# Kernel optimization log

Measured on AMD Instinct MI355X. Metric: run time of the kernel, lower is better.

The kernel has to match this reference:

```python
import jax, jax.numpy as jnp
import numpy as np

N_NODES = 100000
N_EDGES = 1200000
DIM = 64


def _gcn_layer(h, src, dst, norm, W, b):
    # GCNConv: linear -> gather -> normalize -> scatter-add -> bias
    n = h.shape[0]
    h = h @ W                              # [N, D]
    msg = h[src] * norm[:, None]           # [E+N, D] gathered edge messages
    out = jax.ops.segment_sum(msg, dst, num_segments=n)
    return out + b


def setup_inputs() -> dict:
    key = jax.random.key(0)
    ks = jax.random.split(key, 8)
    s = 1.0 / np.sqrt(DIM)
    return {
        "x": jax.random.normal(ks[0], (N_NODES, DIM), jnp.float32),
        "edge_index": jax.random.randint(ks[1], (2, N_EDGES), 0, N_NODES, dtype=jnp.int32),
        "W1": jax.random.normal(ks[2], (DIM, DIM), jnp.float32) * s,
        "b1": jnp.zeros((DIM,), jnp.float32),
        "W2": jax.random.normal(ks[3], (DIM, DIM), jnp.float32) * s,
        "b2": jnp.zeros((DIM,), jnp.float32),
        "W3": jax.random.normal(ks[4], (DIM, DIM), jnp.float32) * s,
        "b3": jnp.zeros((DIM,), jnp.float32),
    }


def reference(x, edge_index, W1, b1, W2, b2, W3, b3):
    n = x.shape[0]
    loops = jnp.arange(n, dtype=edge_index.dtype)
    src = jnp.concatenate([edge_index[0], loops])   # add self-loops (PyG GCNConv default)
    dst = jnp.concatenate([edge_index[1], loops])
    # symmetric degree normalization: norm_e = d^-1/2[src] * d^-1/2[dst]
    deg = jax.ops.segment_sum(jnp.ones(src.shape, x.dtype), dst, num_segments=n)
    dinv = jnp.where(deg > 0, jax.lax.rsqrt(deg), 0.0)
    norm = dinv[src] * dinv[dst]
    h = jax.nn.relu(_gcn_layer(x, src, dst, norm, W1, b1))   # dropout inactive at eval
    h = jax.nn.relu(_gcn_layer(h, src, dst, norm, W2, b2))
    return _gcn_layer(h, src, dst, norm, W3, b3)
```

## Files before the change

kernel.cpp:

```cpp
#include <hip/hip_runtime.h>
#include <math.h>

#define N_NODES 100000
#define N_EDGES 1200000
#define DIM 64
#define ELL_STRIDE 48
#define BNODES 128
#define NBUCKET ((N_NODES + BNODES - 1) / BNODES)
#define BIN_SHIFT 10
#define NBIN ((N_NODES + 1023) >> 10)
#define BIN_CAP 16384
#define CAP 40
#define BIN_BLOCKS 512
#define EPB ((N_EDGES + BIN_BLOCKS - 1) / BIN_BLOCKS)
#define GEMM_BLOCKS ((N_NODES + 63) / 64)

__device__ __forceinline__ unsigned short f2bf(float f) {
    union { float f; unsigned int u; } v; v.f = f;
    unsigned int r = v.u + 0x7FFF + ((v.u >> 16) & 1);
    return (unsigned short)(r >> 16);
}
__device__ __forceinline__ float bf2f(unsigned short us) {
    return __uint_as_float((unsigned int)us << 16);
}


__global__ void k_init(int* __restrict__ tail) {
    if (threadIdx.x < NBIN) tail[threadIdx.x * 16] = 0;
}


__device__ __forceinline__ void gemm_block(int bid, const float* __restrict__ x,
                                           const float* __restrict__ W,
                                           unsigned short* __restrict__ h,
                                           float4* __restrict__ Xlds) {
    const int tid = threadIdx.x;
    const int lane = tid & 63;

    float wreg[64];
#pragma unroll
    for (int k = 0; k < 64; ++k) wreg[k] = W[k * DIM + lane];

    const int base = bid * 64;
#pragma unroll
    for (int it = 0; it < 4; ++it) {
        int f = tid + it * 256;
        int row = base + (f >> 4);
        if (row >= N_NODES) row = N_NODES - 1;
        Xlds[f] = ((const float4*)x)[row * 16 + (f & 15)];
    }
    __syncthreads();

    const int m0 = (tid >> 6) * 16;
    for (int m = 0; m < 16; ++m) {
        const float4* xr = &Xlds[(m0 + m) * 16];
        float a0 = 0.f, a1 = 0.f, a2 = 0.f, a3 = 0.f;
#pragma unroll
        for (int k4 = 0; k4 < 16; ++k4) {
            float4 xv = xr[k4];
            a0 = fmaf(xv.x, wreg[k4 * 4 + 0], a0);
            a1 = fmaf(xv.y, wreg[k4 * 4 + 1], a1);
            a2 = fmaf(xv.z, wreg[k4 * 4 + 2], a2);
            a3 = fmaf(xv.w, wreg[k4 * 4 + 3], a3);
        }
        int row = base + m0 + m;
        if (row < N_NODES)
            h[(size_t)row * DIM + lane] = f2bf((a0 + a1) + (a2 + a3));
    }
}


__global__ void __launch_bounds__(256) k_pre(const int* __restrict__ ei,
                                             const float* __restrict__ x,
                                             const float* __restrict__ W1,
                                             int* __restrict__ tail,
                                             int2* __restrict__ part,
                                             unsigned short* __restrict__ h) {
    __shared__ __align__(16) char smraw[NBIN * CAP * 8];
    __shared__ int lcnt[NBIN];
    __shared__ int gbase[NBIN];
    __shared__ int gcnt[NBIN];

    if (blockIdx.x < GEMM_BLOCKS) {
        gemm_block(blockIdx.x, x, W1, h, (float4*)smraw);
        return;
    }
    int2* stg = (int2*)smraw;
    const int tid = threadIdx.x;
    for (int i = tid; i < NBIN; i += 256) lcnt[i] = 0;
    __syncthreads();

    const int e0 = (blockIdx.x - GEMM_BLOCKS) * EPB;
    const int eend = (e0 + EPB < N_EDGES) ? e0 + EPB : N_EDGES;
    for (int e = e0 + tid; e < eend; e += 256) {
        int s = ei[e], d = ei[N_EDGES + e];
        int bin = d >> BIN_SHIFT;
        int pos = atomicAdd(&lcnt[bin], 1);
        if (pos < CAP) {
            stg[bin * CAP + pos] = make_int2(s, d);
        } else {
            int gp = atomicAdd(&tail[bin * 16], 1);
            part[(size_t)bin * BIN_CAP + gp] = make_int2(s, d);
        }
    }
    __syncthreads();
    if (tid < NBIN) {
        int c = lcnt[tid]; if (c > CAP) c = CAP;
        gcnt[tid] = c;
        gbase[tid] = c ? atomicAdd(&tail[tid * 16], c) : 0;
    }
    __syncthreads();
    const int wv = tid >> 6, ln = tid & 63;
    for (int b = wv; b < NBIN; b += 4) {
        int c = gcnt[b];
        size_t gbb = (size_t)b * BIN_CAP + gbase[b];
        for (int i = ln; i < c; i += 64)
            part[gbb + i] = stg[b * CAP + i];
    }
}


__global__ void __launch_bounds__(256) k_bucket(const int2* __restrict__ part,
                                                const int* __restrict__ tail,
                                                int* __restrict__ ell,
                                                int* __restrict__ deg,
                                                unsigned short* __restrict__ hA,
                                                unsigned short* __restrict__ hB) {
    __shared__ int lcur[BNODES];
    __shared__ int lell[BNODES * ELL_STRIDE];
    const int bucket = blockIdx.x;
    const int tid = threadIdx.x;

    for (int i = tid; i < BNODES; i += 256) lcur[i] = 0;
    __syncthreads();

    const int bin = bucket >> 3;
    const int n = tail[bin * 16];
    const int2* pb = part + (size_t)bin * BIN_CAP;
    const int node0 = bucket * BNODES;
    for (int i = tid; i < n; i += 256) {
        int2 e = pb[i];
        unsigned ld = (unsigned)(e.y - node0);
        if (ld < BNODES) {
            int pos = atomicAdd(&lcur[ld], 1);
            if (pos < ELL_STRIDE) lell[ld * ELL_STRIDE + pos] = e.x;
        }
    }
    __syncthreads();

    for (int idx = tid; idx < BNODES * ELL_STRIDE; idx += 256) {
        int ln = idx / ELL_STRIDE, sl = idx - ln * ELL_STRIDE;
        int dg = lcur[ln];
        int pe = (dg + 7) & ~7;
        if (pe < 16) pe = 16;
        if (sl >= dg && sl < pe) lell[idx] = N_NODES;
    }
    __syncthreads();

    int4* dst4 = (int4*)(ell + (size_t)bucket * BNODES * ELL_STRIDE);
    const int4* src4 = (const int4*)lell;
    for (int i = tid; i < BNODES * ELL_STRIDE / 4; i += 256) dst4[i] = src4[i];
    for (int i = tid; i < BNODES; i += 256) deg[node0 + i] = lcur[i];

    for (int i = tid; i < BNODES * 8; i += 256) {
        int ln = i >> 3;
        int node = node0 + ln;
        if (node < N_NODES) {
            float dd = rsqrtf((float)(lcur[ln] + 1));
            uint4* p = (uint4*)(hA + (size_t)node * DIM) + (i & 7);
            uint4 v = *p;
            {
                float lo, hi;
                lo = __uint_as_float(v.x << 16) * dd; hi = __uint_as_float(v.x & 0xFFFF0000u) * dd;
                v.x = (unsigned)f2bf(lo) | ((unsigned)f2bf(hi) << 16);
                lo = __uint_as_float(v.y << 16) * dd; hi = __uint_as_float(v.y & 0xFFFF0000u) * dd;
                v.y = (unsigned)f2bf(lo) | ((unsigned)f2bf(hi) << 16);
                lo = __uint_as_float(v.z << 16) * dd; hi = __uint_as_float(v.z & 0xFFFF0000u) * dd;
                v.z = (unsigned)f2bf(lo) | ((unsigned)f2bf(hi) << 16);
                lo = __uint_as_float(v.w << 16) * dd; hi = __uint_as_float(v.w & 0xFFFF0000u) * dd;
                v.w = (unsigned)f2bf(lo) | ((unsigned)f2bf(hi) << 16);
            }
            *p = v;
        }
    }
    if (bucket == 0) {
        if (tid < 8)  ((uint4*)(hA + (size_t)N_NODES * DIM))[tid] = make_uint4(0, 0, 0, 0);
        else if (tid < 16) ((uint4*)(hB + (size_t)N_NODES * DIM))[tid - 8] = make_uint4(0, 0, 0, 0);
    }
}


__global__ void __launch_bounds__(256, 4)
k_gatherW(const unsigned short* __restrict__ h,
          const int* __restrict__ deg,
          const int* __restrict__ ell,
          const float* __restrict__ bvec,
          const float* __restrict__ W,
          unsigned short* __restrict__ hout) {
    __shared__ float sh[64 * 64];
    const int tid = threadIdx.x;
    const int lane = tid & 63;
    const int wv = tid >> 6;
    const int base = blockIdx.x * 64;
    const float bl = bvec[lane];

#pragma unroll 2
    for (int m = 0; m < 16; ++m) {
        int node = base + wv * 16 + m;
        if (node >= N_NODES) node = 0;
        int dg = __builtin_amdgcn_readfirstlane(deg[node]);
        const int* row = ell + (size_t)node * ELL_STRIDE;

        int4 e0 = ((const int4*)row)[0];
        int4 e1 = ((const int4*)row)[1];
        int4 e2 = ((const int4*)row)[2];
        int4 e3 = ((const int4*)row)[3];
        float own = bf2f(h[(size_t)node * DIM + lane]);

        float v0  = bf2f(h[(size_t)e0.x * DIM + lane]);
        float v1  = bf2f(h[(size_t)e0.y * DIM + lane]);
        float v2  = bf2f(h[(size_t)e0.z * DIM + lane]);
        float v3  = bf2f(h[(size_t)e0.w * DIM + lane]);
        float v4  = bf2f(h[(size_t)e1.x * DIM + lane]);
        float v5  = bf2f(h[(size_t)e1.y * DIM + lane]);
        float v6  = bf2f(h[(size_t)e1.z * DIM + lane]);
        float v7  = bf2f(h[(size_t)e1.w * DIM + lane]);
        float v8  = bf2f(h[(size_t)e2.x * DIM + lane]);
        float v9  = bf2f(h[(size_t)e2.y * DIM + lane]);
        float v10 = bf2f(h[(size_t)e2.z * DIM + lane]);
        float v11 = bf2f(h[(size_t)e2.w * DIM + lane]);
        float v12 = bf2f(h[(size_t)e3.x * DIM + lane]);
        float v13 = bf2f(h[(size_t)e3.y * DIM + lane]);
        float v14 = bf2f(h[(size_t)e3.z * DIM + lane]);
        float v15 = bf2f(h[(size_t)e3.w * DIM + lane]);

        float acc = ((own + v0) + (v1 + v2)) + ((v3 + v4) + (v5 + v6))
                  + ((v7 + v8) + (v9 + v10)) + ((v11 + v12) + ((v13 + v14) + v15));

        if (dg > 16) {
            int pe = (dg + 7) & ~7;
            for (int k = 16; k < pe; k += 8) {
                int4 a = *(const int4*)(row + k);
                int4 c = *(const int4*)(row + k + 4);
                float w0 = bf2f(h[(size_t)a.x * DIM + lane]);
                float w1 = bf2f(h[(size_t)a.y * DIM + lane]);
                float w2 = bf2f(h[(size_t)a.z * DIM + lane]);
                float w3 = bf2f(h[(size_t)a.w * DIM + lane]);
                float w4 = bf2f(h[(size_t)c.x * DIM + lane]);
                float w5 = bf2f(h[(size_t)c.y * DIM + lane]);
                float w6 = bf2f(h[(size_t)c.z * DIM + lane]);
                float w7 = bf2f(h[(size_t)c.w * DIM + lane]);
                acc += ((w0 + w1) + (w2 + w3)) + ((w4 + w5) + (w6 + w7));
            }
        }

        float dd = rsqrtf((float)(dg + 1));
        float o = fmaxf(fmaf(acc, dd, bl), 0.f);
        sh[(wv * 16 + m) * 64 + lane] = o;
    }

    float wreg[64];
#pragma unroll
    for (int k = 0; k < 64; ++k) wreg[k] = W[k * DIM + lane];

#pragma unroll 4
    for (int m = 0; m < 16; ++m) {
        const float4* xr = (const float4*)&sh[(wv * 16 + m) * 64];
        float a0 = 0.f, a1 = 0.f, a2 = 0.f, a3 = 0.f;
#pragma unroll
        for (int k4 = 0; k4 < 16; ++k4) {
            float4 xv = xr[k4];
            a0 = fmaf(xv.x, wreg[k4 * 4 + 0], a0);
            a1 = fmaf(xv.y, wreg[k4 * 4 + 1], a1);
            a2 = fmaf(xv.z, wreg[k4 * 4 + 2], a2);
            a3 = fmaf(xv.w, wreg[k4 * 4 + 3], a3);
        }
        int rown = base + wv * 16 + m;
        if (rown < N_NODES) {
            float res = (a0 + a1) + (a2 + a3);
            res *= rsqrtf((float)(deg[rown] + 1));
            hout[(size_t)rown * DIM + lane] = f2bf(res);
        }
    }
}


__global__ void k_gather(const unsigned short* __restrict__ h,
                         const int* __restrict__ deg,
                         const int* __restrict__ ell, const float* __restrict__ b,
                         float* __restrict__ out) {
    int node = blockIdx.x * 4 + (threadIdx.x >> 6);
    const int lane = threadIdx.x & 63;
    int dg = __builtin_amdgcn_readfirstlane(deg[node]);
    const int* row = ell + (size_t)node * ELL_STRIDE;

    int4 e0 = ((const int4*)row)[0];
    int4 e1 = ((const int4*)row)[1];
    int4 e2 = ((const int4*)row)[2];
    int4 e3 = ((const int4*)row)[3];
    float own = bf2f(h[(size_t)node * DIM + lane]);

    float v0  = bf2f(h[(size_t)e0.x * DIM + lane]);
    float v1  = bf2f(h[(size_t)e0.y * DIM + lane]);
    float v2  = bf2f(h[(size_t)e0.z * DIM + lane]);
    float v3  = bf2f(h[(size_t)e0.w * DIM + lane]);
    float v4  = bf2f(h[(size_t)e1.x * DIM + lane]);
    float v5  = bf2f(h[(size_t)e1.y * DIM + lane]);
    float v6  = bf2f(h[(size_t)e1.z * DIM + lane]);
    float v7  = bf2f(h[(size_t)e1.w * DIM + lane]);
    float v8  = bf2f(h[(size_t)e2.x * DIM + lane]);
    float v9  = bf2f(h[(size_t)e2.y * DIM + lane]);
    float v10 = bf2f(h[(size_t)e2.z * DIM + lane]);
    float v11 = bf2f(h[(size_t)e2.w * DIM + lane]);
    float v12 = bf2f(h[(size_t)e3.x * DIM + lane]);
    float v13 = bf2f(h[(size_t)e3.y * DIM + lane]);
    float v14 = bf2f(h[(size_t)e3.z * DIM + lane]);
    float v15 = bf2f(h[(size_t)e3.w * DIM + lane]);

    float acc = ((own + v0) + (v1 + v2)) + ((v3 + v4) + (v5 + v6))
              + ((v7 + v8) + (v9 + v10)) + ((v11 + v12) + ((v13 + v14) + v15));

    if (dg > 16) {
        int pe = (dg + 7) & ~7;
        for (int k = 16; k < pe; k += 8) {
            int4 a = *(const int4*)(row + k);
            int4 c = *(const int4*)(row + k + 4);
            float w0 = bf2f(h[(size_t)a.x * DIM + lane]);
            float w1 = bf2f(h[(size_t)a.y * DIM + lane]);
            float w2 = bf2f(h[(size_t)a.z * DIM + lane]);
            float w3 = bf2f(h[(size_t)a.w * DIM + lane]);
            float w4 = bf2f(h[(size_t)c.x * DIM + lane]);
            float w5 = bf2f(h[(size_t)c.y * DIM + lane]);
            float w6 = bf2f(h[(size_t)c.z * DIM + lane]);
            float w7 = bf2f(h[(size_t)c.w * DIM + lane]);
            acc += ((w0 + w1) + (w2 + w3)) + ((w4 + w5) + (w6 + w7));
        }
    }

    float dd = rsqrtf((float)(dg + 1));
    out[(size_t)node * DIM + lane] = fmaf(acc, dd, b[lane]);
}


extern "C" void kernel_launch(void* const* d_in, const int* in_sizes, int n_in,
                              void* d_out, int out_size, void* d_ws, size_t ws_size,
                              hipStream_t stream) {
    const float* x   = (const float*)d_in[0];
    const int*   ei  = (const int*)d_in[1];
    const float* W1  = (const float*)d_in[2];
    const float* b1  = (const float*)d_in[3];
    const float* W2  = (const float*)d_in[4];
    const float* b2  = (const float*)d_in[5];
    const float* W3  = (const float*)d_in[6];
    const float* b3  = (const float*)d_in[7];
    float* out = (float*)d_out;

    char* ws = (char*)d_ws;
    int*            deg   = (int*)ws;
    int*            tailp = (int*)(ws + 0x70000);
    int*            ell   = (int*)(ws + 0xD00000);
    unsigned short* hbufA = (unsigned short*)(ws + 0x2000000);
    unsigned short* hbufB = (unsigned short*)(ws + 0x2D00000);
    int2*           part  = (int2*)(ws + 0x2D00000);

    k_init<<<1, 128, 0, stream>>>(tailp);

    k_pre<<<GEMM_BLOCKS + BIN_BLOCKS, 256, 0, stream>>>(ei, x, W1, tailp, part, hbufA);
    k_bucket<<<NBUCKET, 256, 0, stream>>>(part, tailp, ell, deg, hbufA, hbufB);

    k_gatherW<<<GEMM_BLOCKS, 256, 0, stream>>>(hbufA, deg, ell, b1, W2, hbufB);
    k_gatherW<<<GEMM_BLOCKS, 256, 0, stream>>>(hbufB, deg, ell, b2, W3, hbufA);
    k_gather<<<N_NODES / 4, 256, 0, stream>>>(hbufA, deg, ell, b3, out);
}
```

Measured before the change: 282.9 us.

## Pack edge pairs into 32-bit words and shrink gatherW blocks to 16 nodes

Binned edges are now stored as one 32-bit word holding a 17-bit source and a 10-bit local destination instead of an int2. This halves the partition buffer traffic in k_pre and k_bucket and the staging shared memory. k_gatherW now handles 16 nodes per block instead of 64, with a smaller shared tile, giving more blocks for load balance and occupancy in exchange for reloading W more often per node. The final gather kernel is renamed.

```diff
diff --git a/kernel.cpp b/kernel.cpp
--- a/kernel.cpp
+++ b/kernel.cpp
@@ -14,6 +14,11 @@
 #define BIN_BLOCKS 512
 #define EPB ((N_EDGES + BIN_BLOCKS - 1) / BIN_BLOCKS)
 #define GEMM_BLOCKS ((N_NODES + 63) / 64)
+#define GW_BLOCKS (N_NODES / 16)
+
+#define PACK(s, dloc) (((unsigned)(dloc) << 17) | (unsigned)(s))
+#define UNPACK_S(p)   ((int)((p) & 0x1FFFF))
+#define UNPACK_D(p)   ((int)((p) >> 17))
 
 __device__ __forceinline__ unsigned short f2bf(float f) {
     union { float f; unsigned int u; } v; v.f = f;
@@ -74,9 +79,9 @@
                                              const float* __restrict__ x,
                                              const float* __restrict__ W1,
                                              int* __restrict__ tail,
-                                             int2* __restrict__ part,
+                                             unsigned* __restrict__ part,
                                              unsigned short* __restrict__ h) {
-    __shared__ __align__(16) char smraw[NBIN * CAP * 8];
+    __shared__ __align__(16) char smraw[16384];
     __shared__ int lcnt[NBIN];
     __shared__ int gbase[NBIN];
     __shared__ int gcnt[NBIN];
@@ -85,7 +90,7 @@
         gemm_block(blockIdx.x, x, W1, h, (float4*)smraw);
         return;
     }
-    int2* stg = (int2*)smraw;
+    unsigned* stg = (unsigned*)smraw;
     const int tid = threadIdx.x;
     for (int i = tid; i < NBIN; i += 256) lcnt[i] = 0;
     __syncthreads();
@@ -95,12 +100,13 @@
     for (int e = e0 + tid; e < eend; e += 256) {
         int s = ei[e], d = ei[N_EDGES + e];
         int bin = d >> BIN_SHIFT;
+        unsigned pk = PACK(s, d & 1023);
         int pos = atomicAdd(&lcnt[bin], 1);
         if (pos < CAP) {
-            stg[bin * CAP + pos] = make_int2(s, d);
+            stg[bin * CAP + pos] = pk;
         } else {
             int gp = atomicAdd(&tail[bin * 16], 1);
-            part[(size_t)bin * BIN_CAP + gp] = make_int2(s, d);
+            part[(size_t)bin * BIN_CAP + gp] = pk;
         }
     }
     __syncthreads();
@@ -120,7 +126,7 @@
 }
 
 
-__global__ void __launch_bounds__(256) k_bucket(const int2* __restrict__ part,
+__global__ void __launch_bounds__(256) k_bucket(const unsigned* __restrict__ part,
                                                 const int* __restrict__ tail,
                                                 int* __restrict__ ell,
                                                 int* __restrict__ deg,
@@ -135,15 +141,16 @@
     __syncthreads();
 
     const int bin = bucket >> 3;
+    const int sub = bucket & 7;
     const int n = tail[bin * 16];
-    const int2* pb = part + (size_t)bin * BIN_CAP;
+    const unsigned* pb = part + (size_t)bin * BIN_CAP;
     const int node0 = bucket * BNODES;
     for (int i = tid; i < n; i += 256) {
-        int2 e = pb[i];
-        unsigned ld = (unsigned)(e.y - node0);
+        unsigned p = pb[i];
+        unsigned ld = (unsigned)(UNPACK_D(p) - (sub << 7));
         if (ld < BNODES) {
             int pos = atomicAdd(&lcur[ld], 1);
-            if (pos < ELL_STRIDE) lell[ld * ELL_STRIDE + pos] = e.x;
+            if (pos < ELL_STRIDE) lell[ld * ELL_STRIDE + pos] = UNPACK_S(p);
         }
     }
     __syncthreads();
@@ -169,17 +176,15 @@
             float dd = rsqrtf((float)(lcur[ln] + 1));
             uint4* p = (uint4*)(hA + (size_t)node * DIM) + (i & 7);
             uint4 v = *p;
-            {
-                float lo, hi;
-                lo = __uint_as_float(v.x << 16) * dd; hi = __uint_as_float(v.x & 0xFFFF0000u) * dd;
-                v.x = (unsigned)f2bf(lo) | ((unsigned)f2bf(hi) << 16);
-                lo = __uint_as_float(v.y << 16) * dd; hi = __uint_as_float(v.y & 0xFFFF0000u) * dd;
-                v.y = (unsigned)f2bf(lo) | ((unsigned)f2bf(hi) << 16);
-                lo = __uint_as_float(v.z << 16) * dd; hi = __uint_as_float(v.z & 0xFFFF0000u) * dd;
-                v.z = (unsigned)f2bf(lo) | ((unsigned)f2bf(hi) << 16);
-                lo = __uint_as_float(v.w << 16) * dd; hi = __uint_as_float(v.w & 0xFFFF0000u) * dd;
-                v.w = (unsigned)f2bf(lo) | ((unsigned)f2bf(hi) << 16);
-            }
+            float lo, hi;
+            lo = __uint_as_float(v.x << 16) * dd; hi = __uint_as_float(v.x & 0xFFFF0000u) * dd;
+            v.x = (unsigned)f2bf(lo) | ((unsigned)f2bf(hi) << 16);
+            lo = __uint_as_float(v.y << 16) * dd; hi = __uint_as_float(v.y & 0xFFFF0000u) * dd;
+            v.y = (unsigned)f2bf(lo) | ((unsigned)f2bf(hi) << 16);
+            lo = __uint_as_float(v.z << 16) * dd; hi = __uint_as_float(v.z & 0xFFFF0000u) * dd;
+            v.z = (unsigned)f2bf(lo) | ((unsigned)f2bf(hi) << 16);
+            lo = __uint_as_float(v.w << 16) * dd; hi = __uint_as_float(v.w & 0xFFFF0000u) * dd;
+            v.w = (unsigned)f2bf(lo) | ((unsigned)f2bf(hi) << 16);
             *p = v;
         }
     }
@@ -197,17 +202,16 @@
           const float* __restrict__ bvec,
           const float* __restrict__ W,
           unsigned short* __restrict__ hout) {
-    __shared__ float sh[64 * 64];
+    __shared__ float sh[16 * 64];
     const int tid = threadIdx.x;
     const int lane = tid & 63;
     const int wv = tid >> 6;
-    const int base = blockIdx.x * 64;
+    const int base = blockIdx.x * 16;
     const float bl = bvec[lane];
 
 #pragma unroll 2
-    for (int m = 0; m < 16; ++m) {
-        int node = base + wv * 16 + m;
-        if (node >= N_NODES) node = 0;
+    for (int m = 0; m < 4; ++m) {
+        int node = base + wv * 4 + m;
         int dg = __builtin_amdgcn_readfirstlane(deg[node]);
         const int* row = ell + (size_t)node * ELL_STRIDE;
 
@@ -256,16 +260,16 @@
 
         float dd = rsqrtf((float)(dg + 1));
         float o = fmaxf(fmaf(acc, dd, bl), 0.f);
-        sh[(wv * 16 + m) * 64 + lane] = o;
+        sh[(wv * 4 + m) * 64 + lane] = o;
     }
 
     float wreg[64];
 #pragma unroll
     for (int k = 0; k < 64; ++k) wreg[k] = W[k * DIM + lane];
 
-#pragma unroll 4
-    for (int m = 0; m < 16; ++m) {
-        const float4* xr = (const float4*)&sh[(wv * 16 + m) * 64];
+#pragma unroll
+    for (int m = 0; m < 4; ++m) {
+        const float4* xr = (const float4*)&sh[(wv * 4 + m) * 64];
         float a0 = 0.f, a1 = 0.f, a2 = 0.f, a3 = 0.f;
 #pragma unroll
         for (int k4 = 0; k4 < 16; ++k4) {
@@ -275,20 +279,18 @@
             a2 = fmaf(xv.z, wreg[k4 * 4 + 2], a2);
             a3 = fmaf(xv.w, wreg[k4 * 4 + 3], a3);
         }
-        int rown = base + wv * 16 + m;
-        if (rown < N_NODES) {
-            float res = (a0 + a1) + (a2 + a3);
-            res *= rsqrtf((float)(deg[rown] + 1));
-            hout[(size_t)rown * DIM + lane] = f2bf(res);
-        }
-    }
-}
-
-
-__global__ void k_gather(const unsigned short* __restrict__ h,
-                         const int* __restrict__ deg,
-                         const int* __restrict__ ell, const float* __restrict__ b,
-                         float* __restrict__ out) {
+        int rown = base + wv * 4 + m;
+        float res = (a0 + a1) + (a2 + a3);
+        res *= rsqrtf((float)(deg[rown] + 1));
+        hout[(size_t)rown * DIM + lane] = f2bf(res);
+    }
+}
+
+
+__global__ void k_gatherF(const unsigned short* __restrict__ h,
+                          const int* __restrict__ deg,
+                          const int* __restrict__ ell, const float* __restrict__ b,
+                          float* __restrict__ out) {
     int node = blockIdx.x * 4 + (threadIdx.x >> 6);
     const int lane = threadIdx.x & 63;
     int dg = __builtin_amdgcn_readfirstlane(deg[node]);
@@ -361,14 +363,14 @@
     int*            ell   = (int*)(ws + 0xD00000);
     unsigned short* hbufA = (unsigned short*)(ws + 0x2000000);
     unsigned short* hbufB = (unsigned short*)(ws + 0x2D00000);
-    int2*           part  = (int2*)(ws + 0x2D00000);
+    unsigned*       part  = (unsigned*)(ws + 0x2D00000);
 
     k_init<<<1, 128, 0, stream>>>(tailp);
 
     k_pre<<<GEMM_BLOCKS + BIN_BLOCKS, 256, 0, stream>>>(ei, x, W1, tailp, part, hbufA);
     k_bucket<<<NBUCKET, 256, 0, stream>>>(part, tailp, ell, deg, hbufA, hbufB);
 
-    k_gatherW<<<GEMM_BLOCKS, 256, 0, stream>>>(hbufA, deg, ell, b1, W2, hbufB);
-    k_gatherW<<<GEMM_BLOCKS, 256, 0, stream>>>(hbufB, deg, ell, b2, W3, hbufA);
-    k_gather<<<N_NODES / 4, 256, 0, stream>>>(hbufA, deg, ell, b3, out);
-}
+    k_gatherW<<<GW_BLOCKS, 256, 0, stream>>>(hbufA, deg, ell, b1, W2, hbufB);
+    k_gatherW<<<GW_BLOCKS, 256, 0, stream>>>(hbufB, deg, ell, b2, W3, hbufA);
+    k_gatherF<<<N_NODES / 4, 256, 0, stream>>>(hbufA, deg, ell, b3, out);
+}
```

After: 267.5 us. 5.4% less time.
